# Optimization experiments

Measured on AMD Instinct MI355X. Metric: run time of the kernel, lower is better.

The kernel has to match this reference:

```python
import jax, jax.numpy as jnp
import numpy as np

ALPHA = 0.1
THETA = 0.5
LAYERS = 4
N, E, D_IN, H, D_OUT = 100000, 1600000, 128, 128, 128


def setup_inputs() -> dict:
    key = jax.random.key(0)
    ks = jax.random.split(key, 9)
    x = jax.random.normal(ks[0], (N, D_IN), jnp.float32)
    edge_src = jax.random.randint(ks[1], (E,), 0, N, jnp.int32)
    edge_dst = jax.random.randint(ks[2], (E,), 0, N, jnp.int32)
    edge_w = jax.random.uniform(ks[3], (E,), jnp.float32)
    s_in = 1.0 / np.sqrt(D_IN)
    s_h = 1.0 / np.sqrt(H)
    W0 = jax.random.uniform(ks[4], (D_IN, H), jnp.float32, -s_in, s_in)
    b0 = jax.random.uniform(ks[5], (H,), jnp.float32, -s_in, s_in)
    W1 = jax.random.uniform(ks[6], (H, D_OUT), jnp.float32, -s_h, s_h)
    b1 = jax.random.uniform(ks[7], (D_OUT,), jnp.float32, -s_h, s_h)
    glorot = np.sqrt(6.0 / (H + H))
    convW = jax.random.uniform(ks[8], (LAYERS, H, H), jnp.float32, -glorot, glorot)
    return dict(x=x, edge_src=edge_src, edge_dst=edge_dst, edge_w=edge_w,
                W0=W0, b0=b0, W1=W1, b1=b1, convW=convW)


def reference(x, edge_src, edge_dst, edge_w, W0, b0, W1, b1, convW):
    # input projection + relu; x_0 is the initial residual (GCNII)
    h = jax.nn.relu(x @ W0 + b0)
    x0 = h
    for l in range(LAYERS):
        beta = float(np.log(THETA / (l + 1) + 1.0))
        # SpMM: agg[i] = sum_{(j->i) in E} w_e * h[j]
        msg = h[edge_src] * edge_w[:, None]                      # [E, H]
        agg = jax.ops.segment_sum(msg, edge_dst, num_segments=N)  # [N, H]
        out = (1.0 - ALPHA) * agg + ALPHA * x0                    # initial residual
        out = (1.0 - beta) * out + beta * (out @ convW[l])        # identity mapping
        h = jax.nn.relu(out)
    logits = h @ W1 + b1
    return jax.nn.log_softmax(logits, axis=-1)
```

## Files before the change

### kernel.cpp

```cpp
#include <hip/hip_runtime.h>
#include <math.h>

typedef unsigned int uint;
typedef unsigned short ushort;
typedef unsigned char uchar;
using bf8   = __attribute__((ext_vector_type(8))) short;
using f32x4 = __attribute__((ext_vector_type(4))) float;
using f32x2 = __attribute__((ext_vector_type(2))) float;

__device__ inline ushort f2bf(float f) {
  uint u = __float_as_uint(f);
  return (ushort)((u + 0x7fffu + ((u >> 16) & 1u)) >> 16);
}
__device__ inline float bf2f(ushort s) { return __uint_as_float(((uint)s) << 16); }
__device__ inline uint packbf2(float a, float b) {
  uint ua = __float_as_uint(a), ub = __float_as_uint(b);
  ua = (ua + 0x7fffu + ((ua >> 16) & 1u)) >> 16;
  ub = (ub + 0x7fffu + ((ub >> 16) & 1u)) & 0xffff0000u;
  return ua | ub;
}
__device__ inline float bflo(uint u) { return __uint_as_float(u << 16); }
__device__ inline float bfhi(uint u) { return __uint_as_float(u & 0xffff0000u); }

#if __has_builtin(__builtin_amdgcn_cvt_pk_f32_fp8)
template<bool W>
__device__ inline f32x2 fp8x2_f32(uint v) {
  return __builtin_amdgcn_cvt_pk_f32_fp8((int)v, W);
}
#else
__device__ inline float fp8_1(uint b) {
  uint e = (b >> 3) & 15u, m = b & 7u;
  float nrm = __uint_as_float(((e + 120u) << 23) | (m << 20));
  float sub = (float)m * 0.001953125f;
  return e ? nrm : sub;
}
template<bool W>
__device__ inline f32x2 fp8x2_f32(uint v) {
  uint sh = W ? 16u : 0u;
  f32x2 r; r.x = fp8_1((v >> sh) & 0xffu); r.y = fp8_1((v >> (sh + 8)) & 0xffu);
  return r;
}
#endif

__device__ inline uint f32_fp8(float f) {
  if (!(f > 0.f)) return 0u;
  if (f >= 446.f) return 0x7eu;
  if (f < 0.015625f) return (uint)(f * 512.f + 0.5f);
  uint u = __float_as_uint(f);
  uint r = u + 0x7ffffu + ((u >> 20) & 1u);
  uint eb = r >> 23, mant = (r >> 20) & 7u;
  if (eb > 135u || (eb == 135u && mant == 7u)) return 0x7eu;
  return ((eb - 120u) << 3) | mant;
}

__global__ void hist_k(const int* __restrict__ dst, int* __restrict__ cnt, int E) {
  int tid = blockIdx.x * blockDim.x + threadIdx.x;
  int stride4 = gridDim.x * blockDim.x * 4;
  for (int base = tid * 4; base + 3 < E; base += stride4) {
    int4 d = *(const int4*)&dst[base];
    atomicAdd(&cnt[d.x], 1);
    atomicAdd(&cnt[d.y], 1);
    atomicAdd(&cnt[d.z], 1);
    atomicAdd(&cnt[d.w], 1);
  }
  int tail0 = (E & ~3);
  int e = tail0 + tid;
  if (e < E) atomicAdd(&cnt[dst[e]], 1);
}

__global__ __launch_bounds__(256) void scanA_k(const int* __restrict__ cnt,
                                               int* __restrict__ bsum, int N) {
  __shared__ int red[256];
  int tid = threadIdx.x;
  int i0 = blockIdx.x * 1024 + tid * 4;
  int s = 0;
  #pragma unroll
  for (int k = 0; k < 4; ++k) { int i = i0 + k; if (i < N) s += cnt[i]; }
  red[tid] = s;
  __syncthreads();
  for (int off = 128; off; off >>= 1) {
    if (tid < off) red[tid] += red[tid + off];
    __syncthreads();
  }
  if (tid == 0) bsum[blockIdx.x] = red[0];
}

__global__ __launch_bounds__(128) void scanB_k(const int* __restrict__ bsum,
                                               int* __restrict__ bbase, int nb) {
  __shared__ int buf[2][128];
  int tid = threadIdx.x;
  buf[0][tid] = (tid < nb) ? bsum[tid] : 0;
  __syncthreads();
  int pin = 0;
  for (int off = 1; off < 128; off <<= 1) {
    int x = buf[pin][tid];
    if (tid >= off) x += buf[pin][tid - off];
    buf[1 - pin][tid] = x;
    __syncthreads();
    pin = 1 - pin;
  }
  if (tid < nb) bbase[tid] = (tid == 0) ? 0 : buf[pin][tid - 1];
}

__global__ __launch_bounds__(256) void scanC_k(const int* __restrict__ cnt,
    const int* __restrict__ bbase, int* __restrict__ rp, int N, int E) {
  __shared__ int buf[2][256];
  int tid = threadIdx.x;
  int i0 = blockIdx.x * 1024 + tid * 4;
  int c[4]; int s = 0;
  #pragma unroll
  for (int k = 0; k < 4; ++k) { int i = i0 + k; c[k] = (i < N) ? cnt[i] : 0; s += c[k]; }
  buf[0][tid] = s;
  __syncthreads();
  int pin = 0;
  for (int off = 1; off < 256; off <<= 1) {
    int x = buf[pin][tid];
    if (tid >= off) x += buf[pin][tid - off];
    buf[1 - pin][tid] = x;
    __syncthreads();
    pin = 1 - pin;
  }
  int run = bbase[blockIdx.x] + buf[pin][tid] - s;
  #pragma unroll
  for (int k = 0; k < 4; ++k) {
    int i = i0 + k;
    if (i < N) { rp[i] = run; run += c[k]; }
  }
  if (blockIdx.x == 0 && tid == 0) rp[N] = E;
}

__global__ __launch_bounds__(256) void scatter_k(const int* __restrict__ src,
    const int* __restrict__ dst, const float* __restrict__ w,
    const int* __restrict__ rp, int* __restrict__ cnt,
    uint* __restrict__ epk, int E, int N) {
  int part = blockIdx.x & 7;
  int slice = blockIdx.x >> 3;
  int nslices = gridDim.x >> 3;
  int per = (E + nslices - 1) / nslices;
  int lo = slice * per, hi = min(E, lo + per);
  int nper = (N + 7) >> 3;
  int nlo = part * nper, nhi = min(N, nlo + nper);
  for (int e = lo + threadIdx.x; e < hi; e += 256) {
    int d = dst[e];
    if (d < nlo || d >= nhi) continue;
    int off = atomicAdd(&cnt[d], -1) - 1;
    uint wq = (uint)(w[e] * 32767.f + 0.5f);
    epk[rp[d] + off] = ((uint)src[e] << 15) | wq;
  }
}

__global__ __launch_bounds__(256) void prepW_k(const float* __restrict__ W0,
    const float* __restrict__ convW, const float* __restrict__ W1,
    ushort* __restrict__ Wt) {
  int b = blockIdx.x;
  int m = b >> 4;
  int n0 = (b & 15) * 8;
  const float* W = (m == 0) ? W0 : (m <= 4) ? (convW + (size_t)(m - 1) * 128 * 128) : W1;
  ushort* dst = Wt + (size_t)m * 128 * 128;
  int t = threadIdx.x;
  int n = n0 + (t >> 5);
  int k0 = (t & 31) * 4;
  float a = W[(size_t)(k0 + 0) * 128 + n];
  float c = W[(size_t)(k0 + 1) * 128 + n];
  float d = W[(size_t)(k0 + 2) * 128 + n];
  float e = W[(size_t)(k0 + 3) * 128 + n];
  *(uint2*)&dst[(size_t)n * 128 + k0] = make_uint2(packbf2(a, c), packbf2(d, e));
}

__global__ __launch_bounds__(256) void spmm_k(const int* __restrict__ rp,
    const uint* __restrict__ epk, const uchar* __restrict__ h8,
    const ushort* __restrict__ x0bf, ushort* __restrict__ outbf, int N) {
  int node = (blockIdx.x * blockDim.x + threadIdx.x) >> 4;
  int l16 = threadIdx.x & 15;
  if (node >= N) return;
  int b = rp[node], e = rp[node + 1];
  float a0 = 0.f, a1 = 0.f, a2 = 0.f, a3 = 0.f;
  float a4 = 0.f, a5 = 0.f, a6 = 0.f, a7 = 0.f;
  const uint2* hb = (const uint2*)h8;
#define EDG(EU, HV) do { \
    float wgt = (float)((EU) & 0x7fffu) * (1.f / 32767.f); \
    f32x2 p0 = fp8x2_f32<false>((HV).x), p1 = fp8x2_f32<true>((HV).x); \
    f32x2 p2 = fp8x2_f32<false>((HV).y), p3 = fp8x2_f32<true>((HV).y); \
    a0 = fmaf(wgt, p0.x, a0); a1 = fmaf(wgt, p0.y, a1); \
    a2 = fmaf(wgt, p1.x, a2); a3 = fmaf(wgt, p1.y, a3); \
    a4 = fmaf(wgt, p2.x, a4); a5 = fmaf(wgt, p2.y, a5); \
    a6 = fmaf(wgt, p3.x, a6); a7 = fmaf(wgt, p3.y, a7); \
  } while (0)
  int j = b;
  for (; j + 7 < e; j += 8) {
    uint u0 = epk[j],     u1 = epk[j + 1], u2 = epk[j + 2], u3 = epk[j + 3];
    uint u4 = epk[j + 4], u5 = epk[j + 5], u6 = epk[j + 6], u7 = epk[j + 7];
    uint2 h0 = hb[(size_t)(u0 >> 15) * 16 + l16];
    uint2 h1 = hb[(size_t)(u1 >> 15) * 16 + l16];
    uint2 h2 = hb[(size_t)(u2 >> 15) * 16 + l16];
    uint2 h3 = hb[(size_t)(u3 >> 15) * 16 + l16];
    uint2 h4 = hb[(size_t)(u4 >> 15) * 16 + l16];
    uint2 h5 = hb[(size_t)(u5 >> 15) * 16 + l16];
    uint2 h6 = hb[(size_t)(u6 >> 15) * 16 + l16];
    uint2 h7 = hb[(size_t)(u7 >> 15) * 16 + l16];
    EDG(u0, h0); EDG(u1, h1); EDG(u2, h2); EDG(u3, h3);
    EDG(u4, h4); EDG(u5, h5); EDG(u6, h6); EDG(u7, h7);
  }
  for (; j + 3 < e; j += 4) {
    uint u0 = epk[j], u1 = epk[j + 1], u2 = epk[j + 2], u3 = epk[j + 3];
    uint2 h0 = hb[(size_t)(u0 >> 15) * 16 + l16];
    uint2 h1 = hb[(size_t)(u1 >> 15) * 16 + l16];
    uint2 h2 = hb[(size_t)(u2 >> 15) * 16 + l16];
    uint2 h3 = hb[(size_t)(u3 >> 15) * 16 + l16];
    EDG(u0, h0); EDG(u1, h1); EDG(u2, h2); EDG(u3, h3);
  }
  for (; j < e; ++j) {
    uint u0 = epk[j];
    uint2 h0 = hb[(size_t)(u0 >> 15) * 16 + l16];
    EDG(u0, h0);
  }
#undef EDG
  uint4 xv = ((const uint4*)x0bf)[(size_t)node * 16 + l16];
  float o0 = 0.9f * a0 + 0.1f * bflo(xv.x);
  float o1 = 0.9f * a1 + 0.1f * bfhi(xv.x);
  float o2 = 0.9f * a2 + 0.1f * bflo(xv.y);
  float o3 = 0.9f * a3 + 0.1f * bfhi(xv.y);
  float o4 = 0.9f * a4 + 0.1f * bflo(xv.z);
  float o5 = 0.9f * a5 + 0.1f * bfhi(xv.z);
  float o6 = 0.9f * a6 + 0.1f * bflo(xv.w);
  float o7 = 0.9f * a7 + 0.1f * bfhi(xv.w);
  uint4 u;
  u.x = packbf2(o0, o1); u.y = packbf2(o2, o3);
  u.z = packbf2(o4, o5); u.w = packbf2(o6, o7);
  ((uint4*)outbf)[(size_t)node * 16 + l16] = u;
}

template<int MODE, int ABF, int OUT8>
__global__ __launch_bounds__(256, 4) void gemm_mfma(const void* __restrict__ inv,
    const ushort* __restrict__ Wt, const float* __restrict__ bias,
    float* __restrict__ outf, ushort* __restrict__ outbf, ushort* __restrict__ outbf2,
    uchar* __restrict__ out8, float cin, float cw, int N) {
  const float*  inf = (const float*)inv;
  const ushort* inb = (const ushort*)inv;
  int tid = threadIdx.x;
  int w = tid >> 6, lane = tid & 63;
  int l15 = lane & 15, hi = lane >> 4;
  int rbase = blockIdx.x * 128 + w * 32;

  f32x4 acc[2][8];
  #pragma unroll
  for (int mi = 0; mi < 2; ++mi)
    #pragma unroll
    for (int ni = 0; ni < 8; ++ni)
      acc[mi][ni] = (f32x4){0.f, 0.f, 0.f, 0.f};

  int r0 = min(rbase + l15, N - 1);
  int r1 = min(rbase + 16 + l15, N - 1);

  #pragma unroll
  for (int kt = 0; kt < 4; ++kt) {
    int koff = kt * 32 + hi * 8;
    bf8 a0, a1;
    if (ABF) {
      a0 = *(const bf8*)&inb[(size_t)r0 * 128 + koff];
      a1 = *(const bf8*)&inb[(size_t)r1 * 128 + koff];
    } else {
      float4 f0 = *(const float4*)&inf[(size_t)r0 * 128 + koff];
      float4 f1 = *(const float4*)&inf[(size_t)r0 * 128 + koff + 4];
      float4 g0 = *(const float4*)&inf[(size_t)r1 * 128 + koff];
      float4 g1 = *(const float4*)&inf[(size_t)r1 * 128 + koff + 4];
      union { bf8 v; uint u[4]; } ta, tb;
      ta.u[0] = packbf2(f0.x, f0.y); ta.u[1] = packbf2(f0.z, f0.w);
      ta.u[2] = packbf2(f1.x, f1.y); ta.u[3] = packbf2(f1.z, f1.w);
      tb.u[0] = packbf2(g0.x, g0.y); tb.u[1] = packbf2(g0.z, g0.w);
      tb.u[2] = packbf2(g1.x, g1.y); tb.u[3] = packbf2(g1.z, g1.w);
      a0 = ta.v; a1 = tb.v;
    }
    #pragma unroll
    for (int ni = 0; ni < 8; ++ni) {
      bf8 b = *(const bf8*)&Wt[(size_t)(ni * 16 + l15) * 128 + koff];
      acc[0][ni] = __builtin_amdgcn_mfma_f32_16x16x32_bf16(a0, b, acc[0][ni], 0, 0, 0);
      acc[1][ni] = __builtin_amdgcn_mfma_f32_16x16x32_bf16(a1, b, acc[1][ni], 0, 0, 0);
    }
  }

  float bcol[8];
  if (MODE != 1) {
    #pragma unroll
    for (int ni = 0; ni < 8; ++ni) bcol[ni] = bias[ni * 16 + l15];
  }

  #pragma unroll
  for (int mi = 0; mi < 2; ++mi) {
    #pragma unroll
    for (int reg = 0; reg < 4; ++reg) {
      int row = rbase + mi * 16 + 4 * hi + reg;
      bool valid = (row < N);
      float y[8];
      #pragma unroll
      for (int ni = 0; ni < 8; ++ni) y[ni] = acc[mi][ni][reg];
      if (MODE == 1) {
        if (valid) {
          #pragma unroll
          for (int ni = 0; ni < 8; ++ni) {
            float iv = bf2f(inb[(size_t)row * 128 + ni * 16 + l15]);
            y[ni] = fmaxf(cin * iv + cw * y[ni], 0.f);
          }
        }
      } else {
        #pragma unroll
        for (int ni = 0; ni < 8; ++ni) y[ni] += bcol[ni];
        if (MODE == 0) {
          #pragma unroll
          for (int ni = 0; ni < 8; ++ni) y[ni] = fmaxf(y[ni], 0.f);
        }
      }
      if (MODE == 2) {
        float m = y[0];
        #pragma unroll
        for (int ni = 1; ni < 8; ++ni) m = fmaxf(m, y[ni]);
        #pragma unroll
        for (int off = 1; off <= 8; off <<= 1) m = fmaxf(m, __shfl_xor(m, off));
        float s = 0.f;
        #pragma unroll
        for (int ni = 0; ni < 8; ++ni) s += expf(y[ni] - m);
        #pragma unroll
        for (int off = 1; off <= 8; off <<= 1) s += __shfl_xor(s, off);
        float lg = m + logf(s);
        #pragma unroll
        for (int ni = 0; ni < 8; ++ni) y[ni] -= lg;
      }
      if (valid) {
        if (MODE == 2) {
          #pragma unroll
          for (int ni = 0; ni < 8; ++ni)
            outf[(size_t)row * 128 + ni * 16 + l15] = y[ni];
        } else {
          #pragma unroll
          for (int ni = 0; ni < 8; ++ni) {
            size_t idx = (size_t)row * 128 + ni * 16 + l15;
            if (OUT8) out8[idx] = (uchar)f32_fp8(y[ni]);
            else      outbf[idx] = f2bf(y[ni]);
            if (MODE == 0) outbf2[idx] = f2bf(y[ni]);
          }
        }
      }
    }
  }
}

extern "C" void kernel_launch(void* const* d_in, const int* in_sizes, int n_in,
                              void* d_out, int out_size, void* d_ws, size_t ws_size,
                              hipStream_t stream) {
  const float* x     = (const float*)d_in[0];
  const int*   esrc  = (const int*)d_in[1];
  const int*   edst  = (const int*)d_in[2];
  const float* ew    = (const float*)d_in[3];
  const float* W0    = (const float*)d_in[4];
  const float* b0    = (const float*)d_in[5];
  const float* W1    = (const float*)d_in[6];
  const float* b1    = (const float*)d_in[7];
  const float* convW = (const float*)d_in[8];
  int N = in_sizes[0] / 128;
  int E = in_sizes[1];
  float* outp = (float*)d_out;

  char* ws = (char*)d_ws;
  size_t off = 0;
  auto alloc = [&](size_t bytes) {
    void* p = ws + off;
    off += (bytes + 255) & ~(size_t)255;
    return p;
  };
  uchar*  h8    = (uchar*)alloc((size_t)N * 128);
  ushort* x0bf  = (ushort*)alloc((size_t)N * 128 * 2);
  ushort* bufB  = (ushort*)alloc((size_t)N * 128 * 2);
  ushort* bufA  = (ushort*)alloc((size_t)N * 128 * 2);
  ushort* Wtg   = (ushort*)alloc((size_t)6 * 128 * 128 * 2);
  int*    rp    = (int*)alloc((size_t)(N + 1) * 4);
  int*    cnt   = (int*)alloc((size_t)N * 4);
  uint*   epk   = (uint*)alloc((size_t)E * 4);
  int nbScan = (N + 1023) / 1024;
  int*    bsum  = (int*)alloc((size_t)nbScan * 4);
  int*    bbase = (int*)alloc((size_t)nbScan * 4);

  (void)hipMemsetAsync(cnt, 0, (size_t)N * 4, stream);
  hist_k<<<2048, 256, 0, stream>>>(edst, cnt, E);
  prepW_k<<<96, 256, 0, stream>>>(W0, convW, W1, Wtg);
  scanA_k<<<nbScan, 256, 0, stream>>>(cnt, bsum, N);
  scanB_k<<<1, 128, 0, stream>>>(bsum, bbase, nbScan);
  scanC_k<<<nbScan, 256, 0, stream>>>(cnt, bbase, rp, N, E);
  scatter_k<<<2048, 256, 0, stream>>>(esrc, edst, ew, rp, cnt, epk, E, N);

  int gemmBlocks = (N + 127) / 128;
  int spmmBlocks = (N + 15) / 16;

  gemm_mfma<0, 0, 1><<<gemmBlocks, 256, 0, stream>>>(
      x, Wtg, b0, nullptr, nullptr, x0bf, h8, 0.f, 1.f, N);

  for (int l = 0; l < 4; ++l) {
    float beta = logf(0.5f / (float)(l + 1) + 1.f);
    spmm_k<<<spmmBlocks, 256, 0, stream>>>(rp, epk, h8, x0bf, bufB, N);
    if (l < 3) {
      gemm_mfma<1, 1, 1><<<gemmBlocks, 256, 0, stream>>>(
          bufB, Wtg + (size_t)(1 + l) * 128 * 128, nullptr,
          nullptr, nullptr, nullptr, h8, 1.f - beta, beta, N);
    } else {
      gemm_mfma<1, 1, 0><<<gemmBlocks, 256, 0, stream>>>(
          bufB, Wtg + (size_t)(1 + l) * 128 * 128, nullptr,
          nullptr, bufA, nullptr, nullptr, 1.f - beta, beta, N);
    }
  }

  gemm_mfma<2, 1, 0><<<gemmBlocks, 256, 0, stream>>>(
      bufA, Wtg + (size_t)5 * 128 * 128, b1, outp, nullptr, nullptr, nullptr, 0.f, 1.f, N);
}
```

Baseline: 495.4 us.

## Split feature dim into four column panels so SpMM gathers fit in cache

Stores the fp8 hidden features, x0 and the SpMM output in a panel-major layout of four 32-column slices. SpMM becomes four passes, one per slice, so each pass's random gather touches a 3.2 MB working set that can stay cache-resident. The GEMMs read and write the tiled layout. In exchange, edge indices and weights are re-read four times, each gather is only 4 bytes per lane, and one thread now covers a quarter as many columns.

```diff
diff --git a/kernel.cpp b/kernel.cpp
--- a/kernel.cpp
+++ b/kernel.cpp
@@ -21,6 +21,10 @@
 }
 __device__ inline float bflo(uint u) { return __uint_as_float(u << 16); }
 __device__ inline float bfhi(uint u) { return __uint_as_float(u & 0xffff0000u); }
+
+__device__ inline size_t tix(size_t n32, int row, int c) {
+  return (size_t)(c >> 5) * n32 + (size_t)row * 32 + (c & 31);
+}
 
 #if __has_builtin(__builtin_amdgcn_cvt_pk_f32_fp8)
 template<bool W>
@@ -169,74 +173,70 @@
 
 __global__ __launch_bounds__(256) void spmm_k(const int* __restrict__ rp,
     const uint* __restrict__ epk, const uchar* __restrict__ h8,
-    const ushort* __restrict__ x0bf, ushort* __restrict__ outbf, int N) {
-  int node = (blockIdx.x * blockDim.x + threadIdx.x) >> 4;
-  int l16 = threadIdx.x & 15;
+    const ushort* __restrict__ x0bf, ushort* __restrict__ outbf,
+    int N, int blocksPerPass) {
+  int pass = blockIdx.x / blocksPerPass;
+  int nblk = blockIdx.x - pass * blocksPerPass;
+  int node = (nblk * 256 + threadIdx.x) >> 3;
+  int l8 = threadIdx.x & 7;
   if (node >= N) return;
+  size_t n32 = (size_t)N * 32;
+  const uint* hp = (const uint*)(h8 + (size_t)pass * n32);
   int b = rp[node], e = rp[node + 1];
   float a0 = 0.f, a1 = 0.f, a2 = 0.f, a3 = 0.f;
-  float a4 = 0.f, a5 = 0.f, a6 = 0.f, a7 = 0.f;
-  const uint2* hb = (const uint2*)h8;
 #define EDG(EU, HV) do { \
     float wgt = (float)((EU) & 0x7fffu) * (1.f / 32767.f); \
-    f32x2 p0 = fp8x2_f32<false>((HV).x), p1 = fp8x2_f32<true>((HV).x); \
-    f32x2 p2 = fp8x2_f32<false>((HV).y), p3 = fp8x2_f32<true>((HV).y); \
+    f32x2 p0 = fp8x2_f32<false>(HV), p1 = fp8x2_f32<true>(HV); \
     a0 = fmaf(wgt, p0.x, a0); a1 = fmaf(wgt, p0.y, a1); \
     a2 = fmaf(wgt, p1.x, a2); a3 = fmaf(wgt, p1.y, a3); \
-    a4 = fmaf(wgt, p2.x, a4); a5 = fmaf(wgt, p2.y, a5); \
-    a6 = fmaf(wgt, p3.x, a6); a7 = fmaf(wgt, p3.y, a7); \
   } while (0)
   int j = b;
   for (; j + 7 < e; j += 8) {
     uint u0 = epk[j],     u1 = epk[j + 1], u2 = epk[j + 2], u3 = epk[j + 3];
     uint u4 = epk[j + 4], u5 = epk[j + 5], u6 = epk[j + 6], u7 = epk[j + 7];
-    uint2 h0 = hb[(size_t)(u0 >> 15) * 16 + l16];
-    uint2 h1 = hb[(size_t)(u1 >> 15) * 16 + l16];
-    uint2 h2 = hb[(size_t)(u2 >> 15) * 16 + l16];
-    uint2 h3 = hb[(size_t)(u3 >> 15) * 16 + l16];
-    uint2 h4 = hb[(size_t)(u4 >> 15) * 16 + l16];
-    uint2 h5 = hb[(size_t)(u5 >> 15) * 16 + l16];
-    uint2 h6 = hb[(size_t)(u6 >> 15) * 16 + l16];
-    uint2 h7 = hb[(size_t)(u7 >> 15) * 16 + l16];
+    uint h0 = hp[(size_t)(u0 >> 15) * 8 + l8];
+    uint h1 = hp[(size_t)(u1 >> 15) * 8 + l8];
+    uint h2 = hp[(size_t)(u2 >> 15) * 8 + l8];
+    uint h3 = hp[(size_t)(u3 >> 15) * 8 + l8];
+    uint h4 = hp[(size_t)(u4 >> 15) * 8 + l8];
+    uint h5 = hp[(size_t)(u5 >> 15) * 8 + l8];
+    uint h6 = hp[(size_t)(u6 >> 15) * 8 + l8];
+    uint h7 = hp[(size_t)(u7 >> 15) * 8 + l8];
     EDG(u0, h0); EDG(u1, h1); EDG(u2, h2); EDG(u3, h3);
     EDG(u4, h4); EDG(u5, h5); EDG(u6, h6); EDG(u7, h7);
   }
   for (; j + 3 < e; j += 4) {
     uint u0 = epk[j], u1 = epk[j + 1], u2 = epk[j + 2], u3 = epk[j + 3];
-    uint2 h0 = hb[(size_t)(u0 >> 15) * 16 + l16];
-    uint2 h1 = hb[(size_t)(u1 >> 15) * 16 + l16];
-    uint2 h2 = hb[(size_t)(u2 >> 15) * 16 + l16];
-    uint2 h3 = hb[(size_t)(u3 >> 15) * 16 + l16];
+    uint h0 = hp[(size_t)(u0 >> 15) * 8 + l8];
+    uint h1 = hp[(size_t)(u1 >> 15) * 8 + l8];
+    uint h2 = hp[(size_t)(u2 >> 15) * 8 + l8];
+    uint h3 = hp[(size_t)(u3 >> 15) * 8 + l8];
     EDG(u0, h0); EDG(u1, h1); EDG(u2, h2); EDG(u3, h3);
   }
   for (; j < e; ++j) {
     uint u0 = epk[j];
-    uint2 h0 = hb[(size_t)(u0 >> 15) * 16 + l16];
+    uint h0 = hp[(size_t)(u0 >> 15) * 8 + l8];
     EDG(u0, h0);
   }
 #undef EDG
-  uint4 xv = ((const uint4*)x0bf)[(size_t)node * 16 + l16];
+  const ushort* xp = x0bf + (size_t)pass * n32;
+  uint2 xv = *(const uint2*)&xp[(size_t)node * 32 + l8 * 4];
   float o0 = 0.9f * a0 + 0.1f * bflo(xv.x);
   float o1 = 0.9f * a1 + 0.1f * bfhi(xv.x);
   float o2 = 0.9f * a2 + 0.1f * bflo(xv.y);
   float o3 = 0.9f * a3 + 0.1f * bfhi(xv.y);
-  float o4 = 0.9f * a4 + 0.1f * bflo(xv.z);
-  float o5 = 0.9f * a5 + 0.1f * bfhi(xv.z);
-  float o6 = 0.9f * a6 + 0.1f * bflo(xv.w);
-  float o7 = 0.9f * a7 + 0.1f * bfhi(xv.w);
-  uint4 u;
-  u.x = packbf2(o0, o1); u.y = packbf2(o2, o3);
-  u.z = packbf2(o4, o5); u.w = packbf2(o6, o7);
-  ((uint4*)outbf)[(size_t)node * 16 + l16] = u;
-}
-
-template<int MODE, int ABF, int OUT8>
+  ushort* op = outbf + (size_t)pass * n32;
+  *(uint2*)&op[(size_t)node * 32 + l8 * 4] = make_uint2(packbf2(o0, o1), packbf2(o2, o3));
+}
+
+template<int MODE, int ABF, int OUT8, int TIN>
 __global__ __launch_bounds__(256, 4) void gemm_mfma(const void* __restrict__ inv,
     const ushort* __restrict__ Wt, const float* __restrict__ bias,
     float* __restrict__ outf, ushort* __restrict__ outbf, ushort* __restrict__ outbf2,
     uchar* __restrict__ out8, float cin, float cw, int N) {
   const float*  inf = (const float*)inv;
   const ushort* inb = (const ushort*)inv;
+  size_t n32 = (size_t)N * 32;
   int tid = threadIdx.x;
   int w = tid >> 6, lane = tid & 63;
   int l15 = lane & 15, hi = lane >> 4;
@@ -257,8 +257,15 @@
     int koff = kt * 32 + hi * 8;
     bf8 a0, a1;
     if (ABF) {
-      a0 = *(const bf8*)&inb[(size_t)r0 * 128 + koff];
-      a1 = *(const bf8*)&inb[(size_t)r1 * 128 + koff];
+      if (TIN) {
+        size_t i0 = (size_t)kt * n32 + (size_t)r0 * 32 + hi * 8;
+        size_t i1 = (size_t)kt * n32 + (size_t)r1 * 32 + hi * 8;
+        a0 = *(const bf8*)&inb[i0];
+        a1 = *(const bf8*)&inb[i1];
+      } else {
+        a0 = *(const bf8*)&inb[(size_t)r0 * 128 + koff];
+        a1 = *(const bf8*)&inb[(size_t)r1 * 128 + koff];
+      }
     } else {
       float4 f0 = *(const float4*)&inf[(size_t)r0 * 128 + koff];
       float4 f1 = *(const float4*)&inf[(size_t)r0 * 128 + koff + 4];
@@ -298,7 +305,8 @@
         if (valid) {
           #pragma unroll
           for (int ni = 0; ni < 8; ++ni) {
-            float iv = bf2f(inb[(size_t)row * 128 + ni * 16 + l15]);
+            int c = ni * 16 + l15;
+            float iv = bf2f(inb[TIN ? tix(n32, row, c) : ((size_t)row * 128 + c)]);
             y[ni] = fmaxf(cin * iv + cw * y[ni], 0.f);
           }
         }
@@ -333,10 +341,10 @@
         } else {
           #pragma unroll
           for (int ni = 0; ni < 8; ++ni) {
-            size_t idx = (size_t)row * 128 + ni * 16 + l15;
-            if (OUT8) out8[idx] = (uchar)f32_fp8(y[ni]);
-            else      outbf[idx] = f2bf(y[ni]);
-            if (MODE == 0) outbf2[idx] = f2bf(y[ni]);
+            int c = ni * 16 + l15;
+            if (OUT8) out8[tix(n32, row, c)] = (uchar)f32_fp8(y[ni]);
+            else      outbf[(size_t)row * 128 + c] = f2bf(y[ni]);
+            if (MODE == 0) outbf2[tix(n32, row, c)] = f2bf(y[ni]);
           }
         }
       }
@@ -388,25 +396,26 @@
   scatter_k<<<2048, 256, 0, stream>>>(esrc, edst, ew, rp, cnt, epk, E, N);
 
   int gemmBlocks = (N + 127) / 128;
-  int spmmBlocks = (N + 15) / 16;
-
-  gemm_mfma<0, 0, 1><<<gemmBlocks, 256, 0, stream>>>(
+  int blocksPerPass = (N + 31) / 32;
+  int spmmBlocks = 4 * blocksPerPass;
+
+  gemm_mfma<0, 0, 1, 0><<<gemmBlocks, 256, 0, stream>>>(
       x, Wtg, b0, nullptr, nullptr, x0bf, h8, 0.f, 1.f, N);
 
   for (int l = 0; l < 4; ++l) {
     float beta = logf(0.5f / (float)(l + 1) + 1.f);
-    spmm_k<<<spmmBlocks, 256, 0, stream>>>(rp, epk, h8, x0bf, bufB, N);
+    spmm_k<<<spmmBlocks, 256, 0, stream>>>(rp, epk, h8, x0bf, bufB, N, blocksPerPass);
     if (l < 3) {
-      gemm_mfma<1, 1, 1><<<gemmBlocks, 256, 0, stream>>>(
+      gemm_mfma<1, 1, 1, 1><<<gemmBlocks, 256, 0, stream>>>(
           bufB, Wtg + (size_t)(1 + l) * 128 * 128, nullptr,
           nullptr, nullptr, nullptr, h8, 1.f - beta, beta, N);
     } else {
-      gemm_mfma<1, 1, 0><<<gemmBlocks, 256, 0, stream>>>(
+      gemm_mfma<1, 1, 0, 1><<<gemmBlocks, 256, 0, stream>>>(
           bufB, Wtg + (size_t)(1 + l) * 128 * 128, nullptr,
           nullptr, bufA, nullptr, nullptr, 1.f - beta, beta, N);
     }
   }
 
-  gemm_mfma<2, 1, 0><<<gemmBlocks, 256, 0, stream>>>(
+  gemm_mfma<2, 1, 0, 0><<<gemmBlocks, 256, 0, stream>>>(
       bufA, Wtg + (size_t)5 * 128 * 128, b1, outp, nullptr, nullptr, nullptr, 0.f, 1.f, N);
 }
```

After: 566.5 us. 1.14x slower.
